# Kernel optimization log

Hardware: AMD Instinct MI355X
Metric: run time of the kernel (lower is better)

Reference implementation:

```python
import jax, jax.numpy as jnp
import numpy as np

N_HEADS = 16

def setup_inputs() -> dict:
    key = jax.random.key(0)
    ks = jax.random.split(key, 8)
    bs, t, h, dh = 32, 512, 1024, 64
    s = lambda k, shape: jax.random.normal(k, shape, dtype=jnp.float32) * 0.02
    return {
        "x": jax.random.normal(ks[0], (bs, t, h), dtype=jnp.float32),
        "Wq": s(ks[1], (h, h)),
        "bq": s(ks[2], (h,)),
        "Wk": s(ks[3], (h, h)),
        "bk": s(ks[4], (h,)),
        "Wv": s(ks[5], (h, dh)),
        "bv": s(ks[6], (dh,)),
        "Wo": s(ks[7], (dh, h)),
    }

def reference(x, Wq, bq, Wk, bk, Wv, bv, Wo):
    bs, t, h = x.shape
    dh = Wv.shape[1]
    nh = N_HEADS
    # projections (context == x; static_features=None path)
    q = (x @ Wq + bq).reshape(bs, t, nh, dh)   # [b,t,h,d]
    k = (x @ Wk + bk).reshape(bs, t, nh, dh)
    v = x @ Wv + bv                             # shared single-head V: [b,t,d]
    scale = dh ** -0.5
    # per-head scores [b,h,q,k]
    score = jnp.einsum('bqhd,bkhd->bhqk', q, k) * scale
    # causal mask (mask_future_timesteps=True): -inf above diagonal
    mask = jnp.triu(jnp.full((t, t), -jnp.inf, dtype=score.dtype), 1)
    score = score + mask
    prob = jax.nn.softmax(score, axis=-1)       # attn_dropout is identity (p=0)
    # broadcast shared V across heads
    attn_vec = jnp.einsum('bhqk,bkd->bhqd', prob, v)   # [b,h,t,d]
    m_attn_vec = jnp.mean(attn_vec, axis=1)            # head-mean pooling [b,t,d]
    out = m_attn_vec @ Wo                              # out_proj, no bias; out_dropout identity
    return out, attn_vec
```

## Files before the change

kernel.cpp:

```cpp
#include <hip/hip_runtime.h>
#include <hip/hip_bf16.h>
#include <math.h>

#define BS 32
#define TT 512
#define HH 1024
#define NH 16
#define DH 64
#define MM (BS*TT)
#define NCAT 2176

typedef __attribute__((ext_vector_type(8))) __bf16 bf16x8;
typedef __attribute__((ext_vector_type(4))) float  f32x4;

#define QSCALE 0.18033688011112042f

__device__ __forceinline__ void gld16(const void* g, void* l) {
    __builtin_amdgcn_global_load_lds(
        (const __attribute__((address_space(1))) unsigned int*)g,
        (__attribute__((address_space(3))) unsigned int*)l,
        16, 0, 0);
}

__global__ __launch_bounds__(256) void cvt_x(const float* __restrict__ x,
                                             __bf16* __restrict__ xb)
{
    const size_t i = ((size_t)blockIdx.x * 256 + threadIdx.x) * 8;
    float4 a = *(const float4*)(x + i);
    float4 b = *(const float4*)(x + i + 4);
    bf16x8 v;
    v[0] = (__bf16)a.x; v[1] = (__bf16)a.y; v[2] = (__bf16)a.z; v[3] = (__bf16)a.w;
    v[4] = (__bf16)b.x; v[5] = (__bf16)b.y; v[6] = (__bf16)b.z; v[7] = (__bf16)b.w;
    *(bf16x8*)(xb + i) = v;
}

__global__ __launch_bounds__(256) void prep_w(
    const float* __restrict__ Wq, const float* __restrict__ Wk,
    const float* __restrict__ Wv, const float* __restrict__ bq_,
    const float* __restrict__ bk_, const float* __restrict__ bv_,
    __bf16* __restrict__ Wt, float* __restrict__ bias_cat)
{
    __shared__ __align__(16) __bf16 tile[64][72];
    const int tid = threadIdx.x;
    const int n0 = blockIdx.x * 64;
    const int k0 = blockIdx.y * 64;

    const int n_l = tid & 63;
    const int k_b = tid >> 6;
    const int n   = n0 + n_l;
    #pragma unroll
    for (int j = 0; j < 16; ++j) {
        const int k_l = j * 4 + k_b;
        const int k   = k0 + k_l;
        float v;
        if (n < 1024)      v = Wq[(size_t)k * 1024 + n];
        else if (n < 2048) v = Wk[(size_t)k * 1024 + (n - 1024)];
        else if (n < 2112) v = Wv[(size_t)k * 64 + (n - 2048)];
        else               v = 0.f;
        tile[n_l][k_l] = (__bf16)v;
    }
    if (blockIdx.y == 0 && tid < 64) {
        const int nn = n0 + tid;
        bias_cat[nn] = (nn < 1024) ? bq_[nn]
                     : (nn < 2048) ? bk_[nn - 1024]
                     : (nn < 2112) ? bv_[nn - 2048] : 0.f;
    }
    __syncthreads();
    const int n_l2 = tid >> 2;
    const int k_l2 = (tid & 3) * 16;
    __bf16* dst = Wt + (size_t)(n0 + n_l2) * 1024 + k0 + k_l2;
    *(bf16x8*)dst       = *(const bf16x8*)&tile[n_l2][k_l2];
    *(bf16x8*)(dst + 8) = *(const bf16x8*)&tile[n_l2][k_l2 + 8];
}

__global__ __launch_bounds__(256) void gemm_qkv(
    const __bf16* __restrict__ A, const __bf16* __restrict__ B,
    const float* __restrict__ bias_cat,
    __bf16* __restrict__ Qo, __bf16* __restrict__ Ko,
    __bf16* __restrict__ Vt)
{
    __shared__ __align__(16) __bf16 sA[128 * 32];
    __shared__ __align__(16) __bf16 sB[128 * 32];

    const int tid  = threadIdx.x;
    const int wv   = tid >> 6;
    const int ln   = tid & 63;
    const int quad = ln >> 4;
    const int l16  = ln & 15;

    const int orig = blockIdx.y * 17 + blockIdx.x;
    const int swz  = (orig & 7) * 272 + (orig >> 3);
    const int m0 = (swz / 17) * 128;
    const int n0 = (swz % 17) * 128;

    const int rw = (wv & 1) * 64;
    const int cw = (wv >> 1) * 64;

    f32x4 acc[4][4];
    #pragma unroll
    for (int i = 0; i < 4; ++i)
        #pragma unroll
        for (int j = 0; j < 4; ++j) acc[i][j] = f32x4{0, 0, 0, 0};

    const int srow = wv * 16 + (ln >> 2);
    const int scol = (ln & 3) * 8;
    const __bf16* ga0 = A + (size_t)(m0 + srow) * 1024 + scol;
    const __bf16* gb0 = B + (size_t)(n0 + srow) * 1024 + scol;
    __bf16* la0 = sA + wv * 512;
    __bf16* lb0 = sB + wv * 512;

    for (int k0 = 0; k0 < 1024; k0 += 32) {
        gld16(ga0 + k0, la0);
        gld16(ga0 + (size_t)64 * 1024 + k0, la0 + 2048);
        gld16(gb0 + k0, lb0);
        gld16(gb0 + (size_t)64 * 1024 + k0, lb0 + 2048);
        __syncthreads();

        bf16x8 af[4], bfr[4];
        #pragma unroll
        for (int mt = 0; mt < 4; ++mt)
            af[mt] = *(const bf16x8*)&sA[(rw + mt * 16 + l16) * 32 + quad * 8];
        #pragma unroll
        for (int nt = 0; nt < 4; ++nt)
            bfr[nt] = *(const bf16x8*)&sB[(cw + nt * 16 + l16) * 32 + quad * 8];
        #pragma unroll
        for (int mt = 0; mt < 4; ++mt)
            #pragma unroll
            for (int nt = 0; nt < 4; ++nt)
                acc[mt][nt] = __builtin_amdgcn_mfma_f32_16x16x32_bf16(af[mt], bfr[nt], acc[mt][nt], 0, 0, 0);
        __syncthreads();
    }

    #pragma unroll
    for (int mt = 0; mt < 4; ++mt) {
        #pragma unroll
        for (int nt = 0; nt < 4; ++nt) {
            const int colb = n0 + cw + nt * 16 + l16;
            if (colb >= 2112) continue;
            const float bias = bias_cat[colb];
            #pragma unroll
            for (int r = 0; r < 4; ++r) {
                const int row = m0 + rw + mt * 16 + quad * 4 + r;
                const int b = row >> 9, t = row & 511;
                float v = acc[mt][nt][r] + bias;
                if (colb < 1024) {
                    const int h = colb >> 6, d = colb & 63;
                    Qo[(((size_t)(b * NH + h) * TT) + t) * DH + d] = (__bf16)(v * QSCALE);
                } else if (colb < 2048) {
                    const int c = colb - 1024;
                    const int h = c >> 6, d = c & 63;
                    Ko[(((size_t)(b * NH + h) * TT) + t) * DH + d] = (__bf16)v;
                } else {
                    const int d = colb - 2048;
                    Vt[((size_t)(b * DH + d)) * TT + t] = (__bf16)v;
                }
            }
        }
    }
}

__global__ __launch_bounds__(1024) void attn_mfma(
    const __bf16* __restrict__ Q, const __bf16* __restrict__ K,
    const __bf16* __restrict__ Vt, float* __restrict__ attn_vec,
    float* __restrict__ mav)
{
    __shared__ __align__(16) __bf16 sV[64][512];
    __shared__ float smav[32][64];

    const int bid  = blockIdx.x;
    const int qt2  = 15 - (bid >> 5);
    const int b    = bid & 31;
    const int wave = threadIdx.x >> 6;
    const int lane = threadIdx.x & 63;
    const int quad = lane >> 4;
    const int l16  = lane & 15;
    const int bh   = b * NH + wave;
    const int q0   = qt2 << 5;
    const int kend = q0 + 32;

    {
        float* p = &smav[0][0];
        p[threadIdx.x] = 0.f;
        p[threadIdx.x + 1024] = 0.f;
    }

    const __bf16* Vb = Vt + (size_t)b * DH * TT;
    const int svw = wave & 7;
    #pragma unroll
    for (int r = 0; r < 4; ++r) {
        const int row = wave + r * 16;
        gld16(Vb + (size_t)row * TT + ((lane ^ svw) * 8), &sV[row][0]);
    }

    const __bf16* Qbh = Q + (size_t)bh * TT * DH;
    const __bf16* Kbh = K + (size_t)bh * TT * DH;

    const int perm = ((l16 >> 2) << 3) + (l16 & 3);
    const __bf16* kp1 = Kbh + (size_t)perm * DH;
    const __bf16* kp2 = Kbh + (size_t)(perm + 4) * DH;

    const bf16x8 qA_lo = *(const bf16x8*)(Qbh + (size_t)(q0 + l16) * DH + quad * 8);
    const bf16x8 qA_hi = *(const bf16x8*)(Qbh + (size_t)(q0 + l16) * DH + 32 + quad * 8);
    const bf16x8 qB_lo = *(const bf16x8*)(Qbh + (size_t)(q0 + 16 + l16) * DH + quad * 8);
    const bf16x8 qB_hi = *(const bf16x8*)(Qbh + (size_t)(q0 + 16 + l16) * DH + 32 + quad * 8);

    f32x4 OA[4] = {f32x4{0,0,0,0}, f32x4{0,0,0,0}, f32x4{0,0,0,0}, f32x4{0,0,0,0}};
    f32x4 OB[4] = {f32x4{0,0,0,0}, f32x4{0,0,0,0}, f32x4{0,0,0,0}, f32x4{0,0,0,0}};
    float lA = 0.f, lB = 0.f;

    bf16x8 c1a = *(const bf16x8*)(kp1 + quad * 8);
    bf16x8 c1b = *(const bf16x8*)(kp1 + 32 + quad * 8);
    bf16x8 c2a = *(const bf16x8*)(kp2 + quad * 8);
    bf16x8 c2b = *(const bf16x8*)(kp2 + 32 + quad * 8);
    const int kb1 = (32 < kend) ? 32 : 0;
    bf16x8 n1a = *(const bf16x8*)(kp1 + (size_t)kb1 * DH + quad * 8);
    bf16x8 n1b = *(const bf16x8*)(kp1 + (size_t)kb1 * DH + 32 + quad * 8);
    bf16x8 n2a = *(const bf16x8*)(kp2 + (size_t)kb1 * DH + quad * 8);
    bf16x8 n2b = *(const bf16x8*)(kp2 + (size_t)kb1 * DH + 32 + quad * 8);

    const int sx = l16 & 7;

    __syncthreads();

    for (int kb0 = 0; kb0 < kend; kb0 += 32) {
        const int vg = (((kb0 >> 3) + quad) ^ sx) * 8;
        bf16x8 vf0 = *(const bf16x8*)&sV[l16][vg];
        bf16x8 vf1 = *(const bf16x8*)&sV[16 + l16][vg];
        bf16x8 vf2 = *(const bf16x8*)&sV[32 + l16][vg];
        bf16x8 vf3 = *(const bf16x8*)&sV[48 + l16][vg];

        f32x4 s1A = __builtin_amdgcn_mfma_f32_16x16x32_bf16(c1a, qA_lo, f32x4{0,0,0,0}, 0, 0, 0);
        s1A       = __builtin_amdgcn_mfma_f32_16x16x32_bf16(c1b, qA_hi, s1A, 0, 0, 0);
        f32x4 s2A = __builtin_amdgcn_mfma_f32_16x16x32_bf16(c2a, qA_lo, f32x4{0,0,0,0}, 0, 0, 0);
        s2A       = __builtin_amdgcn_mfma_f32_16x16x32_bf16(c2b, qA_hi, s2A, 0, 0, 0);
        f32x4 s1B = __builtin_amdgcn_mfma_f32_16x16x32_bf16(c1a, qB_lo, f32x4{0,0,0,0}, 0, 0, 0);
        s1B       = __builtin_amdgcn_mfma_f32_16x16x32_bf16(c1b, qB_hi, s1B, 0, 0, 0);
        f32x4 s2B = __builtin_amdgcn_mfma_f32_16x16x32_bf16(c2a, qB_lo, f32x4{0,0,0,0}, 0, 0, 0);
        s2B       = __builtin_amdgcn_mfma_f32_16x16x32_bf16(c2b, qB_hi, s2B, 0, 0, 0);

        if (kb0 == q0) {
            const int qqA = q0 + l16, qqB = q0 + 16 + l16;
            #pragma unroll
            for (int r = 0; r < 4; ++r) {
                const int key1 = kb0 + quad * 8 + r;
                const int key2 = key1 + 4;
                if (key1 > qqA) s1A[r] = -INFINITY;
                if (key2 > qqA) s2A[r] = -INFINITY;
                if (key1 > qqB) s1B[r] = -INFINITY;
                if (key2 > qqB) s2B[r] = -INFINITY;
            }
        }

        bf16x8 pfA, pfB;
        float psA = 0.f, psB = 0.f;
        #pragma unroll
        for (int r = 0; r < 4; ++r) {
            float pa0 = exp2f(s1A[r]);
            float pa1 = exp2f(s2A[r]);
            float pb0 = exp2f(s1B[r]);
            float pb1 = exp2f(s2B[r]);
            psA += pa0 + pa1;
            psB += pb0 + pb1;
            pfA[r]     = (__bf16)pa0;
            pfA[4 + r] = (__bf16)pa1;
            pfB[r]     = (__bf16)pb0;
            pfB[4 + r] = (__bf16)pb1;
        }
        lA += psA;
        lB += psB;

        OA[0] = __builtin_amdgcn_mfma_f32_16x16x32_bf16(pfA, vf0, OA[0], 0, 0, 0);
        OB[0] = __builtin_amdgcn_mfma_f32_16x16x32_bf16(pfB, vf0, OB[0], 0, 0, 0);
        OA[1] = __builtin_amdgcn_mfma_f32_16x16x32_bf16(pfA, vf1, OA[1], 0, 0, 0);
        OB[1] = __builtin_amdgcn_mfma_f32_16x16x32_bf16(pfB, vf1, OB[1], 0, 0, 0);
        OA[2] = __builtin_amdgcn_mfma_f32_16x16x32_bf16(pfA, vf2, OA[2], 0, 0, 0);
        OB[2] = __builtin_amdgcn_mfma_f32_16x16x32_bf16(pfB, vf2, OB[2], 0, 0, 0);
        OA[3] = __builtin_amdgcn_mfma_f32_16x16x32_bf16(pfA, vf3, OA[3], 0, 0, 0);
        OB[3] = __builtin_amdgcn_mfma_f32_16x16x32_bf16(pfB, vf3, OB[3], 0, 0, 0);

        c1a = n1a; c1b = n1b; c2a = n2a; c2b = n2b;
        const int kbn = (kb0 + 64 < kend) ? kb0 + 64 : kend - 32;
        const __bf16* nk1 = kp1 + (size_t)kbn * DH;
        const __bf16* nk2 = kp2 + (size_t)kbn * DH;
        n1a = *(const bf16x8*)(nk1 + quad * 8);
        n1b = *(const bf16x8*)(nk1 + 32 + quad * 8);
        n2a = *(const bf16x8*)(nk2 + quad * 8);
        n2b = *(const bf16x8*)(nk2 + 32 + quad * 8);
    }

    lA += __shfl_xor(lA, 16);
    lA += __shfl_xor(lA, 32);
    lB += __shfl_xor(lB, 16);
    lB += __shfl_xor(lB, 32);

    #pragma unroll
    for (int r = 0; r < 4; ++r) {
        const float invA = 1.0f / __shfl(lA, quad * 4 + r);
        const float invB = 1.0f / __shfl(lB, quad * 4 + r);
        const int ltA = quad * 4 + r;
        const int ltB = ltA + 16;
        const int tA = q0 + ltA;
        const int tB = q0 + ltB;
        float* opA = attn_vec + ((size_t)bh * TT + tA) * DH + l16;
        float* opB = attn_vec + ((size_t)bh * TT + tB) * DH + l16;
        #pragma unroll
        for (int nt = 0; nt < 4; ++nt) {
            const float vA = OA[nt][r] * invA;
            const float vB = OB[nt][r] * invB;
            opA[nt * 16] = vA;
            opB[nt * 16] = vB;
            atomicAdd(&smav[ltA][nt * 16 + l16], vA * (1.f / 16.f));
            atomicAdd(&smav[ltB][nt * 16 + l16], vB * (1.f / 16.f));
        }
    }

    __syncthreads();

    if (threadIdx.x < 512) {
        const int row = threadIdx.x >> 4;
        const int d0  = (threadIdx.x & 15) * 4;
        float4 v;
        v.x = smav[row][d0];
        v.y = smav[row][d0 + 1];
        v.z = smav[row][d0 + 2];
        v.w = smav[row][d0 + 3];
        *(float4*)(mav + ((size_t)(b * TT + q0 + row)) * DH + d0) = v;
    }
}

__global__ __launch_bounds__(256) void gemm_out(
    const float* __restrict__ A, const float* __restrict__ B,
    float* __restrict__ C, int M, int N, int K)
{
    __shared__ __align__(16) __bf16 sA[64][32];
    __shared__ __align__(16) __bf16 sB[64][32];

    const int tid  = threadIdx.x;
    const int wave = tid >> 6;
    const int lane = tid & 63;
    const int m0 = blockIdx.y * 64;
    const int n0 = blockIdx.x * 64;

    f32x4 acc[4] = {f32x4{0,0,0,0}, f32x4{0,0,0,0}, f32x4{0,0,0,0}, f32x4{0,0,0,0}};

    const int ar = tid >> 2;
    const int ac = (tid & 3) * 8;
    const int bk = tid >> 3;
    const int bc = (tid & 7) * 8;
    const int quad = lane >> 4;
    const int l16  = lane & 15;

    for (int k0 = 0; k0 < K; k0 += 32) {
        const float* ap = A + (size_t)(m0 + ar) * K + k0 + ac;
        float4 a0 = *(const float4*)ap;
        float4 a1 = *(const float4*)(ap + 4);
        {
            bf16x8 av;
            av[0] = (__bf16)a0.x; av[1] = (__bf16)a0.y; av[2] = (__bf16)a0.z; av[3] = (__bf16)a0.w;
            av[4] = (__bf16)a1.x; av[5] = (__bf16)a1.y; av[6] = (__bf16)a1.z; av[7] = (__bf16)a1.w;
            *(bf16x8*)&sA[ar][ac] = av;
        }
        const float* bp = B + (size_t)(k0 + bk) * N + n0 + bc;
        float4 b0 = *(const float4*)bp;
        float4 b1 = *(const float4*)(bp + 4);
        sB[bc + 0][bk] = (__bf16)b0.x;
        sB[bc + 1][bk] = (__bf16)b0.y;
        sB[bc + 2][bk] = (__bf16)b0.z;
        sB[bc + 3][bk] = (__bf16)b0.w;
        sB[bc + 4][bk] = (__bf16)b1.x;
        sB[bc + 5][bk] = (__bf16)b1.y;
        sB[bc + 6][bk] = (__bf16)b1.z;
        sB[bc + 7][bk] = (__bf16)b1.w;
        __syncthreads();

        bf16x8 afrag = *(const bf16x8*)&sA[wave * 16 + l16][quad * 8];
        #pragma unroll
        for (int tn = 0; tn < 4; ++tn) {
            bf16x8 bfrag = *(const bf16x8*)&sB[tn * 16 + l16][quad * 8];
            acc[tn] = __builtin_amdgcn_mfma_f32_16x16x32_bf16(afrag, bfrag, acc[tn], 0, 0, 0);
        }
        __syncthreads();
    }

    #pragma unroll
    for (int tn = 0; tn < 4; ++tn) {
        #pragma unroll
        for (int r = 0; r < 4; ++r) {
            int row = m0 + wave * 16 + quad * 4 + r;
            int col = n0 + tn * 16 + l16;
            C[(size_t)row * N + col] = acc[tn][r];
        }
    }
}

extern "C" void kernel_launch(void* const* d_in, const int* in_sizes, int n_in,
                              void* d_out, int out_size, void* d_ws, size_t ws_size,
                              hipStream_t stream)
{
    const float* x  = (const float*)d_in[0];
    const float* Wq = (const float*)d_in[1];
    const float* bq = (const float*)d_in[2];
    const float* Wk = (const float*)d_in[3];
    const float* bk = (const float*)d_in[4];
    const float* Wv = (const float*)d_in[5];
    const float* bv = (const float*)d_in[6];
    const float* Wo = (const float*)d_in[7];

    float* out      = (float*)d_out;
    float* attn_vec = out + (size_t)MM * HH;

    char* ws = (char*)d_ws;
    __bf16* xb  = (__bf16*)ws;
    __bf16* Wt  = xb + (size_t)MM * HH;
    float* bias_cat = (float*)(Wt + (size_t)NCAT * HH);
    __bf16* Qb  = (__bf16*)(bias_cat + 2304);
    __bf16* Kb  = Qb + (size_t)MM * HH;
    __bf16* Vt  = Kb + (size_t)MM * HH;
    float*  mav = (float*)xb;

    cvt_x<<<MM * HH / (256 * 8), 256, 0, stream>>>(x, xb);
    prep_w<<<dim3(NCAT / 64, HH / 64), 256, 0, stream>>>(Wq, Wk, Wv, bq, bk, bv, Wt, bias_cat);
    gemm_qkv<<<dim3(NCAT / 128, MM / 128), 256, 0, stream>>>(xb, Wt, bias_cat, Qb, Kb, Vt);
    attn_mfma<<<BS * NH, 1024, 0, stream>>>(Qb, Kb, Vt, attn_vec, mav);
    gemm_out<<<dim3(HH / 64, MM / 64), 256, 0, stream>>>(mav, Wo, out, MM, HH, DH);
}
```

Baseline: 435.0 us.

## Tune attention kernel: raw exp2, setprio around MFMAs, padded smem, balanced tile order

```diff
diff --git a/kernel.cpp b/kernel.cpp
--- a/kernel.cpp
+++ b/kernel.cpp
@@ -14,6 +14,12 @@
 typedef __attribute__((ext_vector_type(4))) float  f32x4;
 
 #define QSCALE 0.18033688011112042f
+
+#if __has_builtin(__builtin_amdgcn_exp2f)
+#define EXP2F(x) __builtin_amdgcn_exp2f(x)
+#else
+#define EXP2F(x) __expf((x) * 0.69314718055994531f)
+#endif
 
 __device__ __forceinline__ void gld16(const void* g, void* l) {
     __builtin_amdgcn_global_load_lds(
@@ -165,10 +171,10 @@
     float* __restrict__ mav)
 {
     __shared__ __align__(16) __bf16 sV[64][512];
-    __shared__ float smav[32][64];
+    __shared__ float smav[32][65];
 
     const int bid  = blockIdx.x;
-    const int qt2  = 15 - (bid >> 5);
+    const int qt2  = (bid < 256) ? (15 - (bid >> 5)) : ((bid - 256) >> 5);
     const int b    = bid & 31;
     const int wave = threadIdx.x >> 6;
     const int lane = threadIdx.x & 63;
@@ -182,6 +188,7 @@
         float* p = &smav[0][0];
         p[threadIdx.x] = 0.f;
         p[threadIdx.x + 1024] = 0.f;
+        if (threadIdx.x < 32) p[threadIdx.x + 2048] = 0.f;
     }
 
     const __bf16* Vb = Vt + (size_t)b * DH * TT;
@@ -229,6 +236,7 @@
         bf16x8 vf2 = *(const bf16x8*)&sV[32 + l16][vg];
         bf16x8 vf3 = *(const bf16x8*)&sV[48 + l16][vg];
 
+        __builtin_amdgcn_s_setprio(1);
         f32x4 s1A = __builtin_amdgcn_mfma_f32_16x16x32_bf16(c1a, qA_lo, f32x4{0,0,0,0}, 0, 0, 0);
         s1A       = __builtin_amdgcn_mfma_f32_16x16x32_bf16(c1b, qA_hi, s1A, 0, 0, 0);
         f32x4 s2A = __builtin_amdgcn_mfma_f32_16x16x32_bf16(c2a, qA_lo, f32x4{0,0,0,0}, 0, 0, 0);
@@ -237,6 +245,7 @@
         s1B       = __builtin_amdgcn_mfma_f32_16x16x32_bf16(c1b, qB_hi, s1B, 0, 0, 0);
         f32x4 s2B = __builtin_amdgcn_mfma_f32_16x16x32_bf16(c2a, qB_lo, f32x4{0,0,0,0}, 0, 0, 0);
         s2B       = __builtin_amdgcn_mfma_f32_16x16x32_bf16(c2b, qB_hi, s2B, 0, 0, 0);
+        __builtin_amdgcn_s_setprio(0);
 
         if (kb0 == q0) {
             const int qqA = q0 + l16, qqB = q0 + 16 + l16;
@@ -252,23 +261,24 @@
         }
 
         bf16x8 pfA, pfB;
-        float psA = 0.f, psB = 0.f;
+        float psA0 = 0.f, psA1 = 0.f, psB0 = 0.f, psB1 = 0.f;
         #pragma unroll
         for (int r = 0; r < 4; ++r) {
-            float pa0 = exp2f(s1A[r]);
-            float pa1 = exp2f(s2A[r]);
-            float pb0 = exp2f(s1B[r]);
-            float pb1 = exp2f(s2B[r]);
-            psA += pa0 + pa1;
-            psB += pb0 + pb1;
+            float pa0 = EXP2F(s1A[r]);
+            float pa1 = EXP2F(s2A[r]);
+            float pb0 = EXP2F(s1B[r]);
+            float pb1 = EXP2F(s2B[r]);
+            psA0 += pa0; psA1 += pa1;
+            psB0 += pb0; psB1 += pb1;
             pfA[r]     = (__bf16)pa0;
             pfA[4 + r] = (__bf16)pa1;
             pfB[r]     = (__bf16)pb0;
             pfB[4 + r] = (__bf16)pb1;
         }
-        lA += psA;
-        lB += psB;
-
+        lA += psA0 + psA1;
+        lB += psB0 + psB1;
+
+        __builtin_amdgcn_s_setprio(1);
         OA[0] = __builtin_amdgcn_mfma_f32_16x16x32_bf16(pfA, vf0, OA[0], 0, 0, 0);
         OB[0] = __builtin_amdgcn_mfma_f32_16x16x32_bf16(pfB, vf0, OB[0], 0, 0, 0);
         OA[1] = __builtin_amdgcn_mfma_f32_16x16x32_bf16(pfA, vf1, OA[1], 0, 0, 0);
@@ -277,6 +287,7 @@
         OB[2] = __builtin_amdgcn_mfma_f32_16x16x32_bf16(pfB, vf2, OB[2], 0, 0, 0);
         OA[3] = __builtin_amdgcn_mfma_f32_16x16x32_bf16(pfA, vf3, OA[3], 0, 0, 0);
         OB[3] = __builtin_amdgcn_mfma_f32_16x16x32_bf16(pfB, vf3, OB[3], 0, 0, 0);
+        __builtin_amdgcn_s_setprio(0);
 
         c1a = n1a; c1b = n1b; c2a = n2a; c2b = n2b;
         const int kbn = (kb0 + 64 < kend) ? kb0 + 64 : kend - 32;
```

Result: no change. 439.2 us (+1.0%).
